# Performance work log

Hardware: AMD Instinct MI355X
Metric: run time of the kernel (lower is better)

Reference implementation:

```python
import jax, jax.numpy as jnp
import numpy as np

M_SIGMA = 1.0 * 0.997 / 3.0  # args.m * 0.997 / 3


def setup_inputs() -> dict:
    key = jax.random.key(0)
    k1, k2 = jax.random.split(key)
    B, D = 64, 512        # batch (sketches+shapes), embedding dim
    P = 256               # points per cloud
    embeddings = jax.random.normal(k1, (B, D), dtype=jnp.float32)
    xyz = jax.random.normal(k2, (B, P, 3), dtype=jnp.float32)
    return {"embeddings": embeddings, "xyz": xyz}


def _chamfer_all_pairs(shapes):
    # shapes: [M, P, 3]. Returns cd[i, j] = chamfer(shapes[i], shapes[j]),
    # chamfer = mean_p min_q ||x_p - y_q||^2 + mean_q min_p ||x_p - y_q||^2
    sq = jnp.sum(shapes * shapes, axis=-1)                  # [M, P]
    inner = jnp.einsum('ipd,jqd->ijpq', shapes, shapes)     # [M, M, P, P]
    d2 = sq[:, None, :, None] + sq[None, :, None, :] - 2.0 * inner
    cd = jnp.min(d2, axis=3).mean(axis=2) + jnp.min(d2, axis=2).mean(axis=2)
    return cd  # [M, M]


def reference(embeddings, xyz):
    # L2-normalize embeddings along feature dim
    emb = embeddings / jnp.linalg.norm(embeddings, axis=1, keepdims=True)
    B = emb.shape[0]
    mb = B // 2
    shapes = xyz[mb:]                                       # [mb, P, 3]
    sketch_feat, shape_feat = emb[:mb], emb[mb:]            # [mb, D] each
    inner_dot = sketch_feat @ shape_feat.T                  # [mb, mb]
    cd = _chamfer_all_pairs(shapes)                         # [mb, mb]
    real_dist = (cd ** 2) / (2.0 * M_SIGMA ** 2)
    p = jax.nn.softmax(-real_dist, axis=1)
    p_hat = jax.nn.softmax(inner_dot, axis=1)               # use_softmax=True
    reg = jnp.mean(jnp.abs(p_hat - p))                      # use_KL=False
    return reg
```

## Files before the change

kernel.cpp:

```cpp
#include <hip/hip_runtime.h>
#include <math.h>


typedef float f32x2 __attribute__((ext_vector_type(2)));

__device__ float g_cdHalf[992];
__device__ float g_dots[1024];
__device__ unsigned int g_counter = 0;

__device__ __forceinline__ float waveReduceSum64(float v) {
    #pragma unroll
    for (int m = 32; m > 0; m >>= 1) v += __shfl_xor(v, m, 64);
    return v;
}

__global__ __launch_bounds__(256, 4) void fused_kernel(const float* __restrict__ emb,
                                                       const float* __restrict__ xyz,
                                                       float* __restrict__ out) {
    const int t = threadIdx.x;
    const int b = blockIdx.x;

    __shared__ __align__(16) float S[4 * 256];
    __shared__ float red[4];
    __shared__ unsigned int ticket;

    if (b < 992) {
        const int pb  = b >> 1;
        const int dir = b & 1;
        int ii = 0, rem = pb;
        while (rem >= (31 - ii)) { rem -= (31 - ii); ++ii; }
        const int jj = ii + 1 + rem;
        const int outer = dir ? jj : ii;
        const int inner = dir ? ii : jj;

        const float* Po = xyz + (32 + outer) * 768;
        const float* Pi = xyz + (32 + inner) * 768;

        const float qx = Pi[3*t], qy = Pi[3*t+1], qz = Pi[3*t+2];
        S[t]       = -2.0f * qx;
        S[t + 256] = -2.0f * qy;
        S[t + 512] = -2.0f * qz;
        S[t + 768] = qx*qx + qy*qy + qz*qz;
        const float px = Po[3*t], py = Po[3*t+1], pz = Po[3*t+2];
        const float pp = px*px + py*py + pz*pz;
        __syncthreads();

        const f32x2 Px = {px, px}, Py = {py, py}, Pz = {pz, pz};
        f32x2 m0 = {3.4e38f, 3.4e38f}, m1 = {3.4e38f, 3.4e38f};

        #pragma unroll 4
        for (int s = 0; s < 256; s += 4) {
            const float4 vx = *(const float4*)&S[s];
            const float4 vy = *(const float4*)&S[s + 256];
            const float4 vz = *(const float4*)&S[s + 512];
            const float4 vw = *(const float4*)&S[s + 768];
            {
                f32x2 e = {vw.x, vw.y};
                e = Pz * (f32x2){vz.x, vz.y} + e;
                e = Py * (f32x2){vy.x, vy.y} + e;
                e = Px * (f32x2){vx.x, vx.y} + e;
                m0.x = fminf(m0.x, e.x); m0.y = fminf(m0.y, e.y);
            }
            {
                f32x2 e = {vw.z, vw.w};
                e = Pz * (f32x2){vz.z, vz.w} + e;
                e = Py * (f32x2){vy.z, vy.w} + e;
                e = Px * (f32x2){vx.z, vx.w} + e;
                m1.x = fminf(m1.x, e.x); m1.y = fminf(m1.y, e.y);
            }
        }
        const float mn = fminf(fminf(m0.x, m0.y), fminf(m1.x, m1.y)) + pp;

        float v = waveReduceSum64(mn);
        if ((t & 63) == 0) red[t >> 6] = v;
        __syncthreads();
        if (t == 0) {
            const float val = (red[0] + red[1] + red[2] + red[3]) * (1.0f / 256.0f);
            __hip_atomic_store(&g_cdHalf[b], val, __ATOMIC_RELAXED, __HIP_MEMORY_SCOPE_AGENT);
        }
    } else {
        const int i = b - 992;
        float* rowi = S;
        const float* Ei = emb + i * 512;
        rowi[t]       = Ei[t];
        rowi[t + 256] = Ei[t + 256];
        __syncthreads();

        const int w    = t >> 6;
        const int lane = t & 63;

        float ni = 0.0f;
        #pragma unroll
        for (int m = 0; m < 8; ++m) { float a = rowi[lane + 64*m]; ni += a*a; }
        ni = waveReduceSum64(ni);

        for (int j = w; j < 32; j += 4) {
            const float* Ej = emb + (32 + j) * 512;
            float dot = 0.0f, nj = 0.0f;
            #pragma unroll
            for (int m = 0; m < 8; ++m) {
                float a  = rowi[lane + 64*m];
                float bv = Ej[lane + 64*m];
                dot += a * bv;
                nj  += bv * bv;
            }
            dot = waveReduceSum64(dot);
            nj  = waveReduceSum64(nj);
            if (lane == 0)
                __hip_atomic_store(&g_dots[i * 32 + j], dot * rsqrtf(ni * nj),
                                   __ATOMIC_RELAXED, __HIP_MEMORY_SCOPE_AGENT);
        }
    }

    asm volatile("s_waitcnt vmcnt(0)" ::: "memory");
    __syncthreads();
    if (t == 0)
        ticket = __hip_atomic_fetch_add(&g_counter, 1u, __ATOMIC_RELAXED,
                                        __HIP_MEMORY_SCOPE_AGENT) & 1023u;
    __syncthreads();
    if (ticket != 1023u) return;

    const int fi = t >> 3;
    const int jb = (t & 7) << 2;
    const float inv_denom = 1.0f / (2.0f * (0.997f / 3.0f) * (0.997f / 3.0f));

    float sv[4], hv[4];
    #pragma unroll
    for (int k = 0; k < 4; ++k) {
        const int j = jb + k;
        float c = 0.0f;
        if (fi != j) {
            const int a  = fi < j ? fi : j;
            const int bb = fi < j ? j : fi;
            const int pq = a * 31 - (a * (a - 1)) / 2 + (bb - a - 1);
            const float c0 = __hip_atomic_load(&g_cdHalf[2*pq],     __ATOMIC_RELAXED, __HIP_MEMORY_SCOPE_AGENT);
            const float c1 = __hip_atomic_load(&g_cdHalf[2*pq + 1], __ATOMIC_RELAXED, __HIP_MEMORY_SCOPE_AGENT);
            c = c0 + c1;
        }
        sv[k] = -(c * c) * inv_denom;
        hv[k] = __hip_atomic_load(&g_dots[fi * 32 + jb + k], __ATOMIC_RELAXED, __HIP_MEMORY_SCOPE_AGENT);
    }

    float mx1 = fmaxf(fmaxf(sv[0], sv[1]), fmaxf(sv[2], sv[3]));
    float mx2 = fmaxf(fmaxf(hv[0], hv[1]), fmaxf(hv[2], hv[3]));
    #pragma unroll
    for (int m = 1; m <= 4; m <<= 1) {
        mx1 = fmaxf(mx1, __shfl_xor(mx1, m, 64));
        mx2 = fmaxf(mx2, __shfl_xor(mx2, m, 64));
    }
    float e1[4], e2[4], sum1 = 0.0f, sum2 = 0.0f;
    #pragma unroll
    for (int k = 0; k < 4; ++k) {
        e1[k] = expf(sv[k] - mx1); sum1 += e1[k];
        e2[k] = expf(hv[k] - mx2); sum2 += e2[k];
    }
    #pragma unroll
    for (int m = 1; m <= 4; m <<= 1) {
        sum1 += __shfl_xor(sum1, m, 64);
        sum2 += __shfl_xor(sum2, m, 64);
    }
    float acc = 0.0f;
    #pragma unroll
    for (int k = 0; k < 4; ++k) acc += fabsf(e2[k] / sum2 - e1[k] / sum1);

    acc = waveReduceSum64(acc);
    if ((t & 63) == 0) red[t >> 6] = acc;
    __syncthreads();
    if (t == 0)
        out[0] = (red[0] + red[1] + red[2] + red[3]) * (1.0f / 1024.0f);
}

extern "C" void kernel_launch(void* const* d_in, const int* in_sizes, int n_in,
                              void* d_out, int out_size, void* d_ws, size_t ws_size,
                              hipStream_t stream) {
    (void)in_sizes; (void)n_in; (void)out_size; (void)d_ws; (void)ws_size;
    const float* emb = (const float*)d_in[0];
    const float* xyz = (const float*)d_in[1];
    float* out = (float*)d_out;

    hipLaunchKernelGGL(fused_kernel, dim3(1024), dim3(256), 0, stream, emb, xyz, out);
}
```

Measured before the change: 75.24 us.

## Map each chamfer pair direction to one wavefront with register-held points

Each chamfer pair direction is now handled by a single 64-lane wave instead of a whole 256-thread block. Each lane keeps four outer points in registers, and the wave streams the inner cloud straight from global memory with wave-uniform addresses and a double-buffered prefetch. This removes the LDS staging and the block-level barriers from the chamfer path, and cuts the grid from 1024 blocks to 256. The embedding dot-product path is likewise split so each wave owns one sketch row and computes all 32 dots serially, at the cost of fewer resident waves per CU and a longer serial loop per wave.

After: 78.22 us. +4.0%, slower.

```diff
diff --git a/kernel.cpp b/kernel.cpp
--- a/kernel.cpp
+++ b/kernel.cpp
@@ -14,94 +14,110 @@
     return v;
 }
 
-__global__ __launch_bounds__(256, 4) void fused_kernel(const float* __restrict__ emb,
-                                                       const float* __restrict__ xyz,
-                                                       float* __restrict__ out) {
+__global__ __launch_bounds__(256) void fused_kernel(const float* __restrict__ emb,
+                                                    const float* __restrict__ xyz,
+                                                    float* __restrict__ out) {
     const int t = threadIdx.x;
     const int b = blockIdx.x;
+    const int w    = t >> 6;
+    const int lane = t & 63;
 
-    __shared__ __align__(16) float S[4 * 256];
     __shared__ float red[4];
     __shared__ unsigned int ticket;
 
-    if (b < 992) {
-        const int pb  = b >> 1;
-        const int dir = b & 1;
+    if (b < 248) {
+        const int pairIdx = __builtin_amdgcn_readfirstlane((b << 2) | w);
+        const int pb  = pairIdx >> 1;
+        const int dir = pairIdx & 1;
         int ii = 0, rem = pb;
         while (rem >= (31 - ii)) { rem -= (31 - ii); ++ii; }
         const int jj = ii + 1 + rem;
         const int outer = dir ? jj : ii;
         const int inner = dir ? ii : jj;
 
-        const float* Po = xyz + (32 + outer) * 768;
-        const float* Pi = xyz + (32 + inner) * 768;
+        const float*  Po = xyz + (32 + outer) * 768;
+        const float4* Q4 = (const float4*)(xyz + (32 + inner) * 768);
 
-        const float qx = Pi[3*t], qy = Pi[3*t+1], qz = Pi[3*t+2];
-        S[t]       = -2.0f * qx;
-        S[t + 256] = -2.0f * qy;
-        S[t + 512] = -2.0f * qz;
-        S[t + 768] = qx*qx + qy*qy + qz*qz;
-        const float px = Po[3*t], py = Po[3*t+1], pz = Po[3*t+2];
-        const float pp = px*px + py*py + pz*pz;
-        __syncthreads();
+        float px[4], py[4], pz[4], pp[4];
+        #pragma unroll
+        for (int k = 0; k < 4; ++k) {
+            const float* P = Po + 3 * (lane + 64 * k);
+            px[k] = P[0]; py[k] = P[1]; pz[k] = P[2];
+            pp[k] = px[k] * px[k] + py[k] * py[k] + pz[k] * pz[k];
+        }
+        const f32x2 X01 = {-2.f * px[0], -2.f * px[1]}, X23 = {-2.f * px[2], -2.f * px[3]};
+        const f32x2 Y01 = {-2.f * py[0], -2.f * py[1]}, Y23 = {-2.f * py[2], -2.f * py[3]};
+        const f32x2 Z01 = {-2.f * pz[0], -2.f * pz[1]}, Z23 = {-2.f * pz[2], -2.f * pz[3]};
 
-        const f32x2 Px = {px, px}, Py = {py, py}, Pz = {pz, pz};
-        f32x2 m0 = {3.4e38f, 3.4e38f}, m1 = {3.4e38f, 3.4e38f};
+        f32x2 m01 = {3.4e38f, 3.4e38f}, m23 = {3.4e38f, 3.4e38f};
 
-        #pragma unroll 4
-        for (int s = 0; s < 256; s += 4) {
-            const float4 vx = *(const float4*)&S[s];
-            const float4 vy = *(const float4*)&S[s + 256];
-            const float4 vz = *(const float4*)&S[s + 512];
-            const float4 vw = *(const float4*)&S[s + 768];
-            {
-                f32x2 e = {vw.x, vw.y};
-                e = Pz * (f32x2){vz.x, vz.y} + e;
-                e = Py * (f32x2){vy.x, vy.y} + e;
-                e = Px * (f32x2){vx.x, vx.y} + e;
-                m0.x = fminf(m0.x, e.x); m0.y = fminf(m0.y, e.y);
-            }
-            {
-                f32x2 e = {vw.z, vw.w};
-                e = Pz * (f32x2){vz.z, vz.w} + e;
-                e = Py * (f32x2){vy.z, vy.w} + e;
-                e = Px * (f32x2){vx.z, vx.w} + e;
-                m1.x = fminf(m1.x, e.x); m1.y = fminf(m1.y, e.y);
-            }
+#define CHAM_PT(QX_, QY_, QZ_) do {                                   \
+            const float qx_ = (QX_), qy_ = (QY_), qz_ = (QZ_);        \
+            const float qw_ = qx_*qx_ + qy_*qy_ + qz_*qz_;            \
+            f32x2 e01 = {qw_, qw_}, e23 = {qw_, qw_};                 \
+            e01 = Z01 * (f32x2){qz_, qz_} + e01;                      \
+            e01 = Y01 * (f32x2){qy_, qy_} + e01;                      \
+            e01 = X01 * (f32x2){qx_, qx_} + e01;                      \
+            e23 = Z23 * (f32x2){qz_, qz_} + e23;                      \
+            e23 = Y23 * (f32x2){qy_, qy_} + e23;                      \
+            e23 = X23 * (f32x2){qx_, qx_} + e23;                      \
+            m01.x = fminf(m01.x, e01.x); m01.y = fminf(m01.y, e01.y); \
+            m23.x = fminf(m23.x, e23.x); m23.y = fminf(m23.y, e23.y); \
+        } while (0)
+
+#define LOADG(A0,A1,A2,A3,A4,A5, gidx) do {                           \
+            const float4* qp_ = Q4 + 6 * (gidx);                      \
+            A0 = qp_[0]; A1 = qp_[1]; A2 = qp_[2];                    \
+            A3 = qp_[3]; A4 = qp_[4]; A5 = qp_[5];                    \
+        } while (0)
+
+#define COMPG(A0,A1,A2,A3,A4,A5) do {                                 \
+            CHAM_PT(A0.x, A0.y, A0.z);                                \
+            CHAM_PT(A0.w, A1.x, A1.y);                                \
+            CHAM_PT(A1.z, A1.w, A2.x);                                \
+            CHAM_PT(A2.y, A2.z, A2.w);                                \
+            CHAM_PT(A3.x, A3.y, A3.z);                                \
+            CHAM_PT(A3.w, A4.x, A4.y);                                \
+            CHAM_PT(A4.z, A4.w, A5.x);                                \
+            CHAM_PT(A5.y, A5.z, A5.w);                                \
+        } while (0)
+
+        float4 a0,a1,a2,a3,a4,a5, c0,c1,c2,c3,c4,c5;
+        LOADG(a0,a1,a2,a3,a4,a5, 0);
+        for (int g = 0; g < 32; g += 2) {
+            LOADG(c0,c1,c2,c3,c4,c5, g + 1);
+            COMPG(a0,a1,a2,a3,a4,a5);
+            if (g + 2 < 32) LOADG(a0,a1,a2,a3,a4,a5, g + 2);
+            COMPG(c0,c1,c2,c3,c4,c5);
         }
-        const float mn = fminf(fminf(m0.x, m0.y), fminf(m1.x, m1.y)) + pp;
+#undef COMPG
+#undef LOADG
+#undef CHAM_PT
 
-        float v = waveReduceSum64(mn);
-        if ((t & 63) == 0) red[t >> 6] = v;
-        __syncthreads();
-        if (t == 0) {
-            const float val = (red[0] + red[1] + red[2] + red[3]) * (1.0f / 256.0f);
-            __hip_atomic_store(&g_cdHalf[b], val, __ATOMIC_RELAXED, __HIP_MEMORY_SCOPE_AGENT);
-        }
+        float ssum = (m01.x + pp[0]) + (m01.y + pp[1]) +
+                     (m23.x + pp[2]) + (m23.y + pp[3]);
+        ssum = waveReduceSum64(ssum);
+        if (lane == 0)
+            __hip_atomic_store(&g_cdHalf[pairIdx], ssum * (1.0f / 256.0f),
+                               __ATOMIC_RELAXED, __HIP_MEMORY_SCOPE_AGENT);
     } else {
-        const int i = b - 992;
-        float* rowi = S;
+        const int i = ((b - 248) << 2) | w;
         const float* Ei = emb + i * 512;
-        rowi[t]       = Ei[t];
-        rowi[t + 256] = Ei[t + 256];
-        __syncthreads();
-
-        const int w    = t >> 6;
-        const int lane = t & 63;
-
+        float ai[8];
+        #pragma unroll
+        for (int m = 0; m < 8; ++m) ai[m] = Ei[lane + 64 * m];
         float ni = 0.0f;
         #pragma unroll
-        for (int m = 0; m < 8; ++m) { float a = rowi[lane + 64*m]; ni += a*a; }
+        for (int m = 0; m < 8; ++m) ni += ai[m] * ai[m];
         ni = waveReduceSum64(ni);
 
-        for (int j = w; j < 32; j += 4) {
+        for (int j = 0; j < 32; ++j) {
             const float* Ej = emb + (32 + j) * 512;
             float dot = 0.0f, nj = 0.0f;
             #pragma unroll
             for (int m = 0; m < 8; ++m) {
-                float a  = rowi[lane + 64*m];
-                float bv = Ej[lane + 64*m];
-                dot += a * bv;
+                const float bv = Ej[lane + 64 * m];
+                dot += ai[m] * bv;
                 nj  += bv * bv;
             }
             dot = waveReduceSum64(dot);
@@ -116,9 +132,9 @@
     __syncthreads();
     if (t == 0)
         ticket = __hip_atomic_fetch_add(&g_counter, 1u, __ATOMIC_RELAXED,
-                                        __HIP_MEMORY_SCOPE_AGENT) & 1023u;
+                                        __HIP_MEMORY_SCOPE_AGENT) & 255u;
     __syncthreads();
-    if (ticket != 1023u) return;
+    if (ticket != 255u) return;
 
     const int fi = t >> 3;
     const int jb = (t & 7) << 2;
@@ -178,5 +194,5 @@
     const float* xyz = (const float*)d_in[1];
     float* out = (float*)d_out;
 
-    hipLaunchKernelGGL(fused_kernel, dim3(1024), dim3(256), 0, stream, emb, xyz, out);
+    hipLaunchKernelGGL(fused_kernel, dim3(256), dim3(256), 0, stream, emb, xyz, out);
 }
```
